# Performance work log

Measured on AMD Instinct MI355X. Metric: run time of the kernel, lower is better.

## Reference

```python
import jax, jax.numpy as jnp
import numpy as np

N, D, E = 100000, 128, 800000

def setup_inputs() -> dict:
    key = jax.random.key(0)
    k1, k2, k3, k4 = jax.random.split(key, 4)
    z = jax.random.normal(k1, (N, D), dtype=jnp.float32)
    edge_index = jax.random.randint(k2, (2, E), 0, N, dtype=jnp.int64)
    # PyTorch-style init scale for Linear layers (kaiming-uniform-ish via normal is fine for a numeric reference)
    W1 = jax.random.normal(k3, (2 * D, D), dtype=jnp.float32) * (1.0 / np.sqrt(2 * D))
    b1 = jnp.zeros((D,), dtype=jnp.float32)
    W2 = jax.random.normal(k4, (D, 1), dtype=jnp.float32) * (1.0 / np.sqrt(D))
    b2 = jnp.zeros((1,), dtype=jnp.float32)
    return {"z": z, "edge_index": edge_index, "W1": W1, "b1": b1, "W2": W2, "b2": b2}

def reference(z, edge_index, W1, b1, W2, b2):
    # row/col gather of node embeddings
    row, col = edge_index[0], edge_index[1]
    # cat([z[row], z[col]]) @ W1 == z[row] @ W1[:D] + z[col] @ W1[D:]
    # -> avoids materializing the [E, 2D] concatenated tensor
    d = z.shape[1]
    h = z[row] @ W1[:d] + z[col] @ W1[d:] + b1          # [E, D]
    h = jax.nn.relu(h)                                   # Dropout(0.1) is identity in eval mode
    out = h @ W2 + b2                                    # [E, 1]
    return out.squeeze(-1)                               # [E]
```

## Files before the change

### kernel.cpp

```cpp
#include <hip/hip_runtime.h>

#define DDIM 128

typedef __bf16 bf16x8 __attribute__((ext_vector_type(8)));
typedef float  floatx4 __attribute__((ext_vector_type(4)));

__global__ __launch_bounds__(256) void precompute_uv_mfma_q8(
    const float* __restrict__ z, const float* __restrict__ W1,
    const float* __restrict__ b1,
    unsigned char* __restrict__ U8, unsigned char* __restrict__ V8,
    float* __restrict__ u_scale, float* __restrict__ v_scale,
    int N, int nchunks)
{
    __shared__ unsigned short WsF[32 * 64 * 8];

    const int t    = threadIdx.x;
    const int lane = t & 63;
    const int w    = t >> 6;
    const int half = blockIdx.x;
    unsigned char* __restrict__ dst8 = half ? V8 : U8;
    float*         __restrict__ dscl = half ? v_scale : u_scale;
    const float*   __restrict__ Wh   = W1 + (size_t)half * DDIM * DDIM;

    {
        const int nlow = lane & 15;
        const int kq   = (lane >> 4) & 3;
        #pragma unroll
        for (int i = 0; i < 8; ++i) {
            const int ntks = w + i * 4;
            const int nt = ntks >> 2, ks = ntks & 3;
            const int n  = nt * 16 + nlow;
            const int kb = ks * 32 + kq * 8;
            float f[8];
            #pragma unroll
            for (int j = 0; j < 8; ++j)
                f[j] = Wh[(kb + j) * DDIM + n];
            unsigned pk[4];
            #pragma unroll
            for (int j = 0; j < 4; ++j)
                asm("v_cvt_pk_bf16_f32 %0, %1, %2"
                    : "=v"(pk[j]) : "v"(f[2 * j]), "v"(f[2 * j + 1]));
            *(uint4*)&WsF[(ntks * 64 + lane) * 8] = *(const uint4*)pk;
        }
    }
    __syncthreads();

    const int mrow = lane & 15;
    const int quad = lane >> 4;

    float bval[8];
    #pragma unroll
    for (int nt = 0; nt < 8; ++nt)
        bval[nt] = (half == 0) ? b1[nt * 16 + mrow] : 0.f;

    for (int chunk = blockIdx.y; chunk < nchunks; chunk += gridDim.y) {
        const int m0 = chunk * 64 + w * 16;

        bf16x8 afrag[4];
        {
            int grow = m0 + mrow; if (grow > N - 1) grow = N - 1;
            const float* zrow = z + (size_t)grow * DDIM;
            #pragma unroll
            for (int ks = 0; ks < 4; ++ks) {
                const int k0 = ks * 32 + quad * 8;
                const float4 x0 = *(const float4*)(zrow + k0);
                const float4 x1 = *(const float4*)(zrow + k0 + 4);
                unsigned pk[4];
                asm("v_cvt_pk_bf16_f32 %0, %1, %2" : "=v"(pk[0]) : "v"(x0.x), "v"(x0.y));
                asm("v_cvt_pk_bf16_f32 %0, %1, %2" : "=v"(pk[1]) : "v"(x0.z), "v"(x0.w));
                asm("v_cvt_pk_bf16_f32 %0, %1, %2" : "=v"(pk[2]) : "v"(x1.x), "v"(x1.y));
                asm("v_cvt_pk_bf16_f32 %0, %1, %2" : "=v"(pk[3]) : "v"(x1.z), "v"(x1.w));
                afrag[ks] = __builtin_bit_cast(bf16x8, *(const uint4*)pk);
            }
        }

        floatx4 acc[8];
        #pragma unroll
        for (int nt = 0; nt < 8; ++nt)
            acc[nt] = (floatx4){bval[nt], bval[nt], bval[nt], bval[nt]};

        #pragma unroll
        for (int ks = 0; ks < 4; ++ks) {
            #pragma unroll
            for (int nt = 0; nt < 8; ++nt) {
                const bf16x8 b = __builtin_bit_cast(bf16x8,
                    *(const uint4*)&WsF[((nt * 4 + ks) * 64 + lane) * 8]);
                acc[nt] = __builtin_amdgcn_mfma_f32_16x16x32_bf16(afrag[ks], b, acc[nt], 0, 0, 0);
            }
        }

        #pragma unroll
        for (int r = 0; r < 4; ++r) {
            float mx = fmaxf(
                fmaxf(fmaxf(fabsf(acc[0][r]), fabsf(acc[1][r])),
                      fmaxf(fabsf(acc[2][r]), fabsf(acc[3][r]))),
                fmaxf(fmaxf(fabsf(acc[4][r]), fabsf(acc[5][r])),
                      fmaxf(fabsf(acc[6][r]), fabsf(acc[7][r]))));
            #pragma unroll
            for (int m = 1; m < 16; m <<= 1)
                mx = fmaxf(mx, __shfl_xor(mx, m, 16));
            mx = fmaxf(mx, 1e-20f);
            const float inv = 127.f * __builtin_amdgcn_rcpf(mx);

            unsigned char bytes[8];
            #pragma unroll
            for (int nt = 0; nt < 8; ++nt) {
                const float fq = fmaf(acc[nt][r], inv, 12583040.0f);
                bytes[nt] = (unsigned char)(__builtin_bit_cast(unsigned, fq) & 0xffu);
            }
            const int grow = chunk * 64 + w * 16 + quad * 4 + r;
            if (grow < N) {
                *(uint2*)&dst8[(size_t)grow * DDIM + mrow * 8] =
                    *(const uint2*)bytes;
                if (mrow == 0) dscl[grow] = mx * (1.f / 127.f);
            }
        }
    }
}

__global__ __launch_bounds__(256) void edge_kernel_i8(
    const int* __restrict__ ei,
    const unsigned char* __restrict__ U8, const unsigned char* __restrict__ V8,
    const float* __restrict__ u_scale, const float* __restrict__ v_scale,
    const float* __restrict__ W2, const float* __restrict__ b2,
    float* __restrict__ out, int E)
{
    const int t  = threadIdx.x;
    const int p  = t & 15;
    const int g0 = (blockIdx.x * 16 + (t >> 4)) * 4;
    if (g0 >= E) return;

    float ww[8];
    #pragma unroll
    for (int j = 0; j < 8; ++j) ww[j] = W2[j * 16 + p];

    int rows[4], cols[4];
    if (g0 + 3 < E) {
        const int4 r4 = *(const int4*)(ei + g0);
        const int4 c4 = *(const int4*)(ei + (size_t)E + g0);
        rows[0]=r4.x; rows[1]=r4.y; rows[2]=r4.z; rows[3]=r4.w;
        cols[0]=c4.x; cols[1]=c4.y; cols[2]=c4.z; cols[3]=c4.w;
    } else {
        #pragma unroll
        for (int i = 0; i < 4; ++i) {
            const int gi = (g0 + i < E) ? (g0 + i) : (E - 1);
            rows[i] = ei[gi];
            cols[i] = ei[(size_t)E + gi];
        }
    }

    uint2 uu[4], vv[4];
    #pragma unroll
    for (int i = 0; i < 4; ++i)
        uu[i] = *(const uint2*)(U8 + (size_t)rows[i] * DDIM + p * 8);
    #pragma unroll
    for (int i = 0; i < 4; ++i)
        vv[i] = *(const uint2*)(V8 + (size_t)cols[i] * DDIM + p * 8);

    float su[4], sv[4];
    #pragma unroll
    for (int i = 0; i < 4; ++i) { su[i] = u_scale[rows[i]]; sv[i] = v_scale[cols[i]]; }

    const float bias = b2[0];

    #pragma unroll
    for (int i = 0; i < 4; ++i) {
        const unsigned ul = uu[i].x, uh = uu[i].y;
        const unsigned vl = vv[i].x, vh = vv[i].y;
        const float c = -128.f * (su[i] + sv[i]);
        float s = 0.f;
        #pragma unroll
        for (int j = 0; j < 4; ++j) {
            const float uf = (float)((ul >> (8 * j)) & 0xffu);
            const float vf = (float)((vl >> (8 * j)) & 0xffu);
            const float h  = fmaf(su[i], uf, fmaf(sv[i], vf, c));
            s = fmaf(fmaxf(h, 0.f), ww[j], s);
        }
        #pragma unroll
        for (int j = 0; j < 4; ++j) {
            const float uf = (float)((uh >> (8 * j)) & 0xffu);
            const float vf = (float)((vh >> (8 * j)) & 0xffu);
            const float h  = fmaf(su[i], uf, fmaf(sv[i], vf, c));
            s = fmaf(fmaxf(h, 0.f), ww[4 + j], s);
        }
        #pragma unroll
        for (int off = 8; off > 0; off >>= 1)
            s += __shfl_down(s, off, 16);
        if (p == 0 && g0 + i < E) out[g0 + i] = s + bias;
    }
}

__global__ __launch_bounds__(256) void edge_fused_fallback(
    const float* __restrict__ z, const int* __restrict__ ei,
    const float* __restrict__ W1, const float* __restrict__ b1,
    const float* __restrict__ W2, const float* __restrict__ b2,
    float* __restrict__ out, int N, int E)
{
    const int tid  = blockIdx.x * 256 + threadIdx.x;
    const int e    = tid >> 6;
    const int lane = tid & 63;
    if (e >= E) return;

    const int row = ei[e];
    const int col = ei[(size_t)E + e];
    const float* zr = z + (size_t)row * DDIM;
    const float* zc = z + (size_t)col * DDIM;

    float h0 = b1[lane];
    float h1 = b1[lane + 64];
    for (int k = 0; k < DDIM; ++k) {
        const float a = zr[k];
        const float b = zc[k];
        h0 = fmaf(a, W1[k * DDIM + lane],               h0);
        h0 = fmaf(b, W1[(DDIM + k) * DDIM + lane],      h0);
        h1 = fmaf(a, W1[k * DDIM + lane + 64],          h1);
        h1 = fmaf(b, W1[(DDIM + k) * DDIM + lane + 64], h1);
    }
    float s = fmaxf(h0, 0.f) * W2[lane] + fmaxf(h1, 0.f) * W2[lane + 64];
    #pragma unroll
    for (int off = 32; off > 0; off >>= 1)
        s += __shfl_down(s, off, 64);
    if (lane == 0) out[e] = s + b2[0];
}

extern "C" void kernel_launch(void* const* d_in, const int* in_sizes, int n_in,
                              void* d_out, int out_size, void* d_ws, size_t ws_size,
                              hipStream_t stream)
{
    const float* z  = (const float*)d_in[0];
    const int*   ei = (const int*)d_in[1];
    const float* W1 = (const float*)d_in[2];
    const float* b1 = (const float*)d_in[3];
    const float* W2 = (const float*)d_in[4];
    const float* b2 = (const float*)d_in[5];
    float*       out = (float*)d_out;

    const int N = in_sizes[0] / DDIM;
    const int E = in_sizes[1] / 2;

    const size_t n128 = (size_t)N * DDIM;
    const size_t need = 2 * n128 + 2 * (size_t)N * sizeof(float) + 256;
    if (ws_size >= need) {
        unsigned char* U8 = (unsigned char*)d_ws;
        unsigned char* V8 = U8 + n128;
        float* usc = (float*)(((size_t)(V8 + n128) + 255) & ~(size_t)255);
        float* vsc = usc + N;
        const int nchunks = (N + 63) / 64;
        const int gy = (nchunks + 3) / 4;
        hipLaunchKernelGGL(precompute_uv_mfma_q8, dim3(2, gy), dim3(256), 0, stream,
                           z, W1, b1, U8, V8, usc, vsc, N, nchunks);
        hipLaunchKernelGGL(edge_kernel_i8, dim3((E + 63) / 64), dim3(256), 0, stream,
                           ei, U8, V8, usc, vsc, W2, b2, out, E);
    } else {
        hipLaunchKernelGGL(edge_fused_fallback, dim3((E + 3) / 4), dim3(256), 0, stream,
                           z, ei, W1, b1, W2, b2, out, N, E);
    }
}
```

Before: 149.7 us.

## Prefetch next z chunk in registers, overlap with W staging, vectorize edge output

The precompute kernel now issues the z-row loads for its first chunk before staging W1 into shared memory, and for each later chunk while the MFMAs of the current one run. This hides global load latency behind other work. The grid is doubled (fewer chunks per block) and launch bounds request 4 blocks per CU. The edge kernel collects its four per-edge results and writes them with one float4 store. The register prefetch buffer adds register pressure and could limit occupancy.

```diff
diff --git a/kernel.cpp b/kernel.cpp
--- a/kernel.cpp
+++ b/kernel.cpp
@@ -5,7 +5,7 @@
 typedef __bf16 bf16x8 __attribute__((ext_vector_type(8)));
 typedef float  floatx4 __attribute__((ext_vector_type(4)));
 
-__global__ __launch_bounds__(256) void precompute_uv_mfma_q8(
+__global__ __launch_bounds__(256, 4) void precompute_uv_mfma_q8(
     const float* __restrict__ z, const float* __restrict__ W1,
     const float* __restrict__ b1,
     unsigned char* __restrict__ U8, unsigned char* __restrict__ V8,
@@ -22,6 +22,25 @@
     float*         __restrict__ dscl = half ? v_scale : u_scale;
     const float*   __restrict__ Wh   = W1 + (size_t)half * DDIM * DDIM;
 
+    const int mrow = lane & 15;
+    const int quad = lane >> 4;
+    const int gy   = gridDim.y;
+
+    float4 rx[8];
+    auto issue_loads = [&](int ch) {
+        int grow = ch * 64 + w * 16 + mrow;
+        if (grow > N - 1) grow = N - 1;
+        const float* zrow = z + (size_t)grow * DDIM;
+        #pragma unroll
+        for (int ks = 0; ks < 4; ++ks) {
+            const int k0 = ks * 32 + quad * 8;
+            rx[2 * ks]     = *(const float4*)(zrow + k0);
+            rx[2 * ks + 1] = *(const float4*)(zrow + k0 + 4);
+        }
+    };
+
+    if (blockIdx.y < nchunks) issue_loads(blockIdx.y);
+
     {
         const int nlow = lane & 15;
         const int kq   = (lane >> 4) & 3;
@@ -43,36 +62,30 @@
             *(uint4*)&WsF[(ntks * 64 + lane) * 8] = *(const uint4*)pk;
         }
     }
-    __syncthreads();
-
-    const int mrow = lane & 15;
-    const int quad = lane >> 4;
 
     float bval[8];
     #pragma unroll
     for (int nt = 0; nt < 8; ++nt)
         bval[nt] = (half == 0) ? b1[nt * 16 + mrow] : 0.f;
 
-    for (int chunk = blockIdx.y; chunk < nchunks; chunk += gridDim.y) {
-        const int m0 = chunk * 64 + w * 16;
-
+    __syncthreads();
+
+    for (int chunk = blockIdx.y; chunk < nchunks; chunk += gy) {
         bf16x8 afrag[4];
-        {
-            int grow = m0 + mrow; if (grow > N - 1) grow = N - 1;
-            const float* zrow = z + (size_t)grow * DDIM;
-            #pragma unroll
-            for (int ks = 0; ks < 4; ++ks) {
-                const int k0 = ks * 32 + quad * 8;
-                const float4 x0 = *(const float4*)(zrow + k0);
-                const float4 x1 = *(const float4*)(zrow + k0 + 4);
-                unsigned pk[4];
-                asm("v_cvt_pk_bf16_f32 %0, %1, %2" : "=v"(pk[0]) : "v"(x0.x), "v"(x0.y));
-                asm("v_cvt_pk_bf16_f32 %0, %1, %2" : "=v"(pk[1]) : "v"(x0.z), "v"(x0.w));
-                asm("v_cvt_pk_bf16_f32 %0, %1, %2" : "=v"(pk[2]) : "v"(x1.x), "v"(x1.y));
-                asm("v_cvt_pk_bf16_f32 %0, %1, %2" : "=v"(pk[3]) : "v"(x1.z), "v"(x1.w));
-                afrag[ks] = __builtin_bit_cast(bf16x8, *(const uint4*)pk);
-            }
-        }
+        #pragma unroll
+        for (int ks = 0; ks < 4; ++ks) {
+            const float4 x0 = rx[2 * ks];
+            const float4 x1 = rx[2 * ks + 1];
+            unsigned pk[4];
+            asm("v_cvt_pk_bf16_f32 %0, %1, %2" : "=v"(pk[0]) : "v"(x0.x), "v"(x0.y));
+            asm("v_cvt_pk_bf16_f32 %0, %1, %2" : "=v"(pk[1]) : "v"(x0.z), "v"(x0.w));
+            asm("v_cvt_pk_bf16_f32 %0, %1, %2" : "=v"(pk[2]) : "v"(x1.x), "v"(x1.y));
+            asm("v_cvt_pk_bf16_f32 %0, %1, %2" : "=v"(pk[3]) : "v"(x1.z), "v"(x1.w));
+            afrag[ks] = __builtin_bit_cast(bf16x8, *(const uint4*)pk);
+        }
+
+        const int nxt = chunk + gy;
+        if (nxt < nchunks) issue_loads(nxt);
 
         floatx4 acc[8];
         #pragma unroll
@@ -163,6 +176,7 @@
 
     const float bias = b2[0];
 
+    float sres[4];
     #pragma unroll
     for (int i = 0; i < 4; ++i) {
         const unsigned ul = uu[i].x, uh = uu[i].y;
@@ -186,7 +200,18 @@
         #pragma unroll
         for (int off = 8; off > 0; off >>= 1)
             s += __shfl_down(s, off, 16);
-        if (p == 0 && g0 + i < E) out[g0 + i] = s + bias;
+        sres[i] = s + bias;
+    }
+
+    if (p == 0) {
+        if (g0 + 3 < E) {
+            float4 o; o.x = sres[0]; o.y = sres[1]; o.z = sres[2]; o.w = sres[3];
+            *(float4*)&out[g0] = o;
+        } else {
+            #pragma unroll
+            for (int i = 0; i < 4; ++i)
+                if (g0 + i < E) out[g0 + i] = sres[i];
+        }
     }
 }
 
@@ -246,7 +271,7 @@
         float* usc = (float*)(((size_t)(V8 + n128) + 255) & ~(size_t)255);
         float* vsc = usc + N;
         const int nchunks = (N + 63) / 64;
-        const int gy = (nchunks + 3) / 4;
+        const int gy = (nchunks + 1) / 2;
         hipLaunchKernelGGL(precompute_uv_mfma_q8, dim3(2, gy), dim3(256), 0, stream,
                            z, W1, b1, U8, V8, usc, vsc, N, nchunks);
         hipLaunchKernelGGL(edge_kernel_i8, dim3((E + 63) / 64), dim3(256), 0, stream,
```

New measurement: 140.1 us. -6.4%, faster.
